# Performance work log

Measured on AMD Instinct MI355X. Metric: run time of the kernel, lower is better.

## Reference

```python
import jax, jax.numpy as jnp
import numpy as np

B, S, D, H = 4, 2048, 1024, 16
DK = D // H


def setup_inputs() -> dict:
    key = jax.random.key(0)
    ks = jax.random.split(key, 12)
    s = 1.0 / np.sqrt(D)
    return {
        "query": jax.random.normal(ks[0], (B, S, D), jnp.float32),
        "key": jax.random.normal(ks[1], (B, S, D), jnp.float32),
        "value": jax.random.normal(ks[2], (B, S, D), jnp.float32),
        "mask": jax.random.randint(ks[3], (B, S), 0, 2, jnp.int32),
        "wq": jax.random.normal(ks[4], (D, D), jnp.float32) * s,
        "bq": jnp.zeros((D,), jnp.float32),
        "wk": jax.random.normal(ks[5], (D, D), jnp.float32) * s,
        "bk": jnp.zeros((D,), jnp.float32),
        "wv": jax.random.normal(ks[6], (D, D), jnp.float32) * s,
        "bv": jnp.zeros((D,), jnp.float32),
        "wo": jax.random.normal(ks[7], (D, D), jnp.float32) * s,
        "bo": jnp.zeros((D,), jnp.float32),
    }


def reference(query, key, value, mask, wq, bq, wk, bk, wv, bv, wo, bo):
    # torch Linear: y = x @ W.T + b
    def proj(x, w, b):
        y = jnp.einsum('bsd,ed->bse', x, w) + b
        return y.reshape(B, S, H, DK).transpose(0, 2, 1, 3)  # [B,H,S,DK]

    q = proj(query, wq, bq)
    k = proj(key, wk, bk)
    v = proj(value, wv, bv)

    scores = jnp.einsum('bhqd,bhkd->bhqk', q, k) / jnp.sqrt(jnp.float32(DK))
    m = mask[:, None, None, :]  # [B,1,1,S_kv]
    scores = jnp.where(m == 0, jnp.float32(-1e9), scores)
    attn = jax.nn.softmax(scores, axis=-1)  # dropout p=0.0 (eval)
    out = jnp.einsum('bhqk,bhkd->bhqd', attn, v)
    out = out.transpose(0, 2, 1, 3).reshape(B, S, D)
    return jnp.einsum('bsd,ed->bse', out, wo) + bo
```

## Files before the change

### kernel.cpp

```cpp
#include <hip/hip_runtime.h>
#include <hip/hip_bf16.h>

typedef __bf16 bf16;
typedef bf16 bf16x2 __attribute__((ext_vector_type(2)));
typedef bf16 bf16x4 __attribute__((ext_vector_type(4)));
typedef bf16 bf16x8 __attribute__((ext_vector_type(8)));
typedef float f32x4 __attribute__((ext_vector_type(4)));
typedef float f32x16 __attribute__((ext_vector_type(16)));
typedef unsigned int u32;
typedef u32 u32x4 __attribute__((ext_vector_type(4)));

#define MFMA16(A,B,C) __builtin_amdgcn_mfma_f32_16x16x32_bf16(A,B,C,0,0,0)
#define MFMA32(A,B,C) __builtin_amdgcn_mfma_f32_32x32x16_bf16(A,B,C,0,0,0)

__device__ __forceinline__ void gld_lds16(const void* g, void* l) {
  __builtin_amdgcn_global_load_lds(
      (const __attribute__((address_space(1))) void*)g,
      (__attribute__((address_space(3))) void*)l, 16, 0, 0);
}

__global__ void cast3_kernel(const float* __restrict__ s0, const float* __restrict__ s1,
                             const float* __restrict__ s2,
                             bf16* __restrict__ d0, bf16* __restrict__ d1, bf16* __restrict__ d2) {
  const int which = blockIdx.x >> 13;
  const int i = (blockIdx.x & 8191) * 256 + threadIdx.x;
  const float* s = which == 0 ? s0 : which == 1 ? s1 : s2;
  bf16* d = which == 0 ? d0 : which == 1 ? d1 : d2;
  float4 v = ((const float4*)s)[i];
  bf16x4 o;
  o[0] = (bf16)v.x; o[1] = (bf16)v.y; o[2] = (bf16)v.z; o[3] = (bf16)v.w;
  *(bf16x4*)(d + (size_t)i * 4) = o;
}

__global__ void cast4_kernel(const float* __restrict__ s0, const float* __restrict__ s1,
                             const float* __restrict__ s2, const float* __restrict__ s3,
                             bf16* __restrict__ d0, bf16* __restrict__ d1,
                             bf16* __restrict__ d2, bf16* __restrict__ d3) {
  const int which = blockIdx.x >> 10;
  const int i = (blockIdx.x & 1023) * 256 + threadIdx.x;
  const float* s = which == 0 ? s0 : which == 1 ? s1 : which == 2 ? s2 : s3;
  bf16* d = which == 0 ? d0 : which == 1 ? d1 : which == 2 ? d2 : d3;
  float4 v = ((const float4*)s)[i];
  bf16x4 o;
  o[0] = (bf16)v.x; o[1] = (bf16)v.y; o[2] = (bf16)v.z; o[3] = (bf16)v.w;
  *(bf16x4*)(d + (size_t)i * 4) = o;
}

__device__ __forceinline__ void gemm256_core(
    const bf16* __restrict__ aBase, const bf16* __restrict__ bBase,
    bf16* sA, bf16* sB, f32x4 (&acc)[8][4])
{
  const int t = threadIdx.x;
  const int lane = t & 63, w = t >> 6;
  const int wr = w >> 2, wc = w & 3;
  const int c = lane & 15, g = lane >> 4;

  const int tl   = (t * 16) ^ (((t >> 3) & 7) << 4);
  const int srow = tl >> 6;
  const int scol = (tl & 63) >> 1;
  const int dstE = t * 8;

  auto stage = [&](int buf, int kt) {
#pragma unroll
    for (int r = 0; r < 2; ++r)
      gld_lds16(aBase + (size_t)(r * 128 + srow) * 1024 + kt * 32 + scol,
                &sA[buf * 8192 + r * 4096 + dstE]);
#pragma unroll
    for (int r = 0; r < 2; ++r)
      gld_lds16(bBase + (size_t)(r * 128 + srow) * 1024 + kt * 32 + scol,
                &sB[buf * 8192 + r * 4096 + dstE]);
  };

  auto rd = [&](const bf16* s, int row) -> bf16x8 {
    const int phys = (row * 64 + g * 16) ^ (((row >> 1) & 7) << 4);
    return *(const bf16x8*)((const char*)s + phys);
  };

  stage(0, 0);
  stage(1, 1);

#pragma unroll 1
  for (int kt = 0; kt < 32; ++kt) {
    __builtin_amdgcn_s_barrier();
    if (kt < 30) {
      stage((kt + 2) % 3, kt + 2);
      asm volatile("s_waitcnt vmcnt(8)" ::: "memory");
    } else if (kt == 30) {
      asm volatile("s_waitcnt vmcnt(4)" ::: "memory");
    } else {
      asm volatile("s_waitcnt vmcnt(0)" ::: "memory");
    }
    __builtin_amdgcn_s_barrier();

    const bf16* tA = sA + (kt % 3) * 8192;
    const bf16* tB = sB + (kt % 3) * 8192;

    bf16x8 bfr[4];
#pragma unroll
    for (int ni = 0; ni < 4; ++ni) bfr[ni] = rd(tB, wc * 64 + ni * 16 + c);
    bf16x8 af[4];
#pragma unroll
    for (int mi = 0; mi < 4; ++mi) af[mi] = rd(tA, wr * 128 + mi * 16 + c);
    __builtin_amdgcn_s_setprio(1);
#pragma unroll
    for (int mi = 0; mi < 4; ++mi)
#pragma unroll
      for (int ni = 0; ni < 4; ++ni)
        acc[mi][ni] = MFMA16(af[mi], bfr[ni], acc[mi][ni]);
    __builtin_amdgcn_s_setprio(0);
#pragma unroll
    for (int mi = 0; mi < 4; ++mi) af[mi] = rd(tA, wr * 128 + (mi + 4) * 16 + c);
    __builtin_amdgcn_s_setprio(1);
#pragma unroll
    for (int mi = 0; mi < 4; ++mi)
#pragma unroll
      for (int ni = 0; ni < 4; ++ni)
        acc[mi + 4][ni] = MFMA16(af[mi], bfr[ni], acc[mi + 4][ni]);
    __builtin_amdgcn_s_setprio(0);
  }
}

__global__ __launch_bounds__(512, 2) void qkv_gemm256(
    const bf16* __restrict__ qx, const bf16* __restrict__ kx, const bf16* __restrict__ vx,
    const bf16* __restrict__ wqb, const bf16* __restrict__ wkb, const bf16* __restrict__ wvb,
    const float* __restrict__ bq, const float* __restrict__ bk, const float* __restrict__ bv,
    bf16* __restrict__ qp, bf16* __restrict__ kp, bf16* __restrict__ vt, float qscale)
{
  __shared__ bf16 sA[3 * 8192];
  __shared__ bf16 sB[3 * 8192];
  const int z = blockIdx.z;
  const bf16* A   = z == 0 ? qx  : z == 1 ? kx  : vx;
  const bf16* Bm  = z == 0 ? wqb : z == 1 ? wkb : wvb;
  const float* bias = z == 0 ? bq : z == 1 ? bk : bv;
  const int bm = blockIdx.y, bn = blockIdx.x;

  f32x4 acc[8][4] = {};
  gemm256_core(A + (size_t)(bm * 256) * 1024, Bm + (size_t)(bn * 256) * 1024, sA, sB, acc);

  const int t = threadIdx.x, lane = t & 63, w = t >> 6;
  const int wr = w >> 2, wc = w & 3, c = lane & 15, g = lane >> 4;
  const float sc = z == 0 ? qscale : 1.0f;
  bf16* Cb = z == 0 ? qp : kp;
#pragma unroll
  for (int ni = 0; ni < 4; ++ni) {
    const int col = bn * 256 + wc * 64 + ni * 16 + c;
    const float bvv = bias[col];
#pragma unroll
    for (int mi = 0; mi < 8; ++mi) {
#pragma unroll
      for (int r4 = 0; r4 < 4; ++r4) {
        const int row = bm * 256 + wr * 128 + mi * 16 + g * 4 + r4;
        const float val = (acc[mi][ni][r4] + bvv) * sc;
        if (z == 2) {
          const int bb = row >> 11, s = row & 2047;
          vt[((size_t)(bb * 1024 + col)) * 2048 + s] = (bf16)val;
        } else {
          Cb[(size_t)row * 1024 + col] = (bf16)val;
        }
      }
    }
  }
}

__global__ __launch_bounds__(512, 2) void out_gemm256(
    const bf16* __restrict__ A, const bf16* __restrict__ Bm,
    const float* __restrict__ bias, float* __restrict__ Cout)
{
  __shared__ bf16 sA[3 * 8192];
  __shared__ bf16 sB[3 * 8192];
  const int bm = blockIdx.y, bn = blockIdx.x;

  f32x4 acc[8][4] = {};
  gemm256_core(A + (size_t)(bm * 256) * 1024, Bm + (size_t)(bn * 256) * 1024, sA, sB, acc);

  const int t = threadIdx.x, lane = t & 63, w = t >> 6;
  const int wr = w >> 2, wc = w & 3, c = lane & 15, g = lane >> 4;
#pragma unroll
  for (int ni = 0; ni < 4; ++ni) {
    const int col = bn * 256 + wc * 64 + ni * 16 + c;
    const float bvv = bias[col];
#pragma unroll
    for (int mi = 0; mi < 8; ++mi) {
#pragma unroll
      for (int r4 = 0; r4 < 4; ++r4) {
        const int row = bm * 256 + wr * 128 + mi * 16 + g * 4 + r4;
        Cout[(size_t)row * 1024 + col] = acc[mi][ni][r4] + bvv;
      }
    }
  }
}

__global__ __launch_bounds__(256) void attn_kernel(
    const bf16* __restrict__ Qp, const bf16* __restrict__ Kp, const bf16* __restrict__ Vt,
    const int* __restrict__ mask, bf16* __restrict__ Out)
{
  __shared__ bf16 sK[2][64 * 64];
  __shared__ bf16 sV[2][64 * 64];

  const int bh = blockIdx.x;
  const int b = bh >> 4, h = bh & 15;
  const int t = threadIdx.x, lane = t & 63, w = t >> 6;
  const int q32 = lane & 31, hi = lane >> 5;
  const int q0 = blockIdx.y * 128 + w * 32;

  const char* kBase = (const char*)(Kp + (size_t)(b * 2048) * 1024 + h * 64);
  const char* vBase = (const char*)(Vt + (size_t)(bh * 64) * 2048);

  auto stageKV = [&](int buf, int kt) {
#pragma unroll
    for (int i = 0; i < 2; ++i) {
      const int idx = i * 256 + t;
      const int row = idx >> 3;
      const int cb = ((t & 7) * 16) ^ ((row & 7) << 4);
      gld_lds16(kBase + (size_t)(kt * 64 + row) * 2048 + cb, (char*)sK[buf] + idx * 16);
      gld_lds16(vBase + (size_t)row * 4096 + kt * 128 + cb, (char*)sV[buf] + idx * 16);
    }
  };

  bf16x8 qf[4];
  const bf16* qrow = Qp + (size_t)(b * 2048 + q0 + q32) * 1024 + h * 64;
#pragma unroll
  for (int ks = 0; ks < 4; ++ks)
    qf[ks] = *(const bf16x8*)&qrow[ks * 16 + hi * 8];

  float mrun = -1e30f, lrun = 0.f;
  f32x16 aco[2] = {};

  const int* mrow = mask + b * 2048;

  stageKV(0, 0);
  __syncthreads();
  int cur = 0;
  for (int kt = 0; kt < 32; ++kt) {
    if (kt + 1 < 32) stageKV(cur ^ 1, kt + 1);

    f32x16 st[2];
#pragma unroll
    for (int kf = 0; kf < 2; ++kf)
#pragma unroll
      for (int q4 = 0; q4 < 4; ++q4) {
        const int4 mm = *(const int4*)&mrow[kt * 64 + kf * 32 + q4 * 8 + hi * 4];
        st[kf][q4 * 4 + 0] = mm.x ? 0.0f : -1e9f;
        st[kf][q4 * 4 + 1] = mm.y ? 0.0f : -1e9f;
        st[kf][q4 * 4 + 2] = mm.z ? 0.0f : -1e9f;
        st[kf][q4 * 4 + 3] = mm.w ? 0.0f : -1e9f;
      }

#pragma unroll
    for (int ks = 0; ks < 4; ++ks) {
      bf16x8 k0f, k1f;
      {
        const int row = q32;
        const int byt = (row * 128 + ks * 32 + hi * 16) ^ ((row & 7) << 4);
        k0f = *(const bf16x8*)((const char*)sK[cur] + byt);
      }
      {
        const int row = 32 + q32;
        const int byt = (row * 128 + ks * 32 + hi * 16) ^ ((row & 7) << 4);
        k1f = *(const bf16x8*)((const char*)sK[cur] + byt);
      }
      __builtin_amdgcn_s_setprio(1);
      st[0] = MFMA32(k0f, qf[ks], st[0]);
      st[1] = MFMA32(k1f, qf[ks], st[1]);
      __builtin_amdgcn_s_setprio(0);
    }

    float t0 = fmaxf(st[0][0], st[0][1]), t1 = fmaxf(st[0][2], st[0][3]);
    float t2 = fmaxf(st[1][0], st[1][1]), t3 = fmaxf(st[1][2], st[1][3]);
#pragma unroll
    for (int i = 4; i < 16; i += 4) {
      t0 = fmaxf(t0, fmaxf(st[0][i], st[0][i + 1]));
      t1 = fmaxf(t1, fmaxf(st[0][i + 2], st[0][i + 3]));
      t2 = fmaxf(t2, fmaxf(st[1][i], st[1][i + 1]));
      t3 = fmaxf(t3, fmaxf(st[1][i + 2], st[1][i + 3]));
    }
    float tmax = fmaxf(fmaxf(t0, t1), fmaxf(t2, t3));
    tmax = fmaxf(tmax, __shfl_xor(tmax, 32, 64));
    if (!__all(tmax <= mrun + 11.5f)) {
      const float mnew = fmaxf(mrun, tmax);
      const float sc = exp2f(mrun - mnew);
      mrun = mnew;
      lrun *= sc;
      aco[0] *= sc;
      aco[1] *= sc;
    }
    float rs0 = 0.f, rs1 = 0.f, rs2 = 0.f, rs3 = 0.f;
#pragma unroll
    for (int i = 0; i < 16; i += 4) {
      float p00 = exp2f(st[0][i] - mrun),     p01 = exp2f(st[0][i + 1] - mrun);
      float p02 = exp2f(st[0][i + 2] - mrun), p03 = exp2f(st[0][i + 3] - mrun);
      float p10 = exp2f(st[1][i] - mrun),     p11 = exp2f(st[1][i + 1] - mrun);
      float p12 = exp2f(st[1][i + 2] - mrun), p13 = exp2f(st[1][i + 3] - mrun);
      st[0][i] = p00; st[0][i + 1] = p01; st[0][i + 2] = p02; st[0][i + 3] = p03;
      st[1][i] = p10; st[1][i + 1] = p11; st[1][i + 2] = p12; st[1][i + 3] = p13;
      rs0 += p00 + p01; rs1 += p02 + p03;
      rs2 += p10 + p11; rs3 += p12 + p13;
    }
    float rs = (rs0 + rs1) + (rs2 + rs3);
    rs += __shfl_xor(rs, 32, 64);
    lrun += rs;

    bf16x8 pa[4];
#pragma unroll
    for (int kf = 0; kf < 2; ++kf) {
      u32 u[4][2];
#pragma unroll
      for (int g2 = 0; g2 < 4; ++g2) {
        asm("v_cvt_pk_bf16_f32 %0, %1, %2"
            : "=v"(u[g2][0]) : "v"(st[kf][4 * g2 + 0]), "v"(st[kf][4 * g2 + 1]));
        asm("v_cvt_pk_bf16_f32 %0, %1, %2"
            : "=v"(u[g2][1]) : "v"(st[kf][4 * g2 + 2]), "v"(st[kf][4 * g2 + 3]));
      }
      u32 d0 = u[0][0], d2 = u[1][0];
      asm("v_permlane32_swap_b32 %0, %1" : "+v"(d0), "+v"(d2));
      u32 d1 = u[0][1], d3 = u[1][1];
      asm("v_permlane32_swap_b32 %0, %1" : "+v"(d1), "+v"(d3));
      u32x4 ud = {d0, d1, d2, d3};
      pa[2 * kf] = __builtin_bit_cast(bf16x8, ud);
      u32 e0 = u[2][0], e2 = u[3][0];
      asm("v_permlane32_swap_b32 %0, %1" : "+v"(e0), "+v"(e2));
      u32 e1 = u[2][1], e3 = u[3][1];
      asm("v_permlane32_swap_b32 %0, %1" : "+v"(e1), "+v"(e3));
      u32x4 ue = {e0, e1, e2, e3};
      pa[2 * kf + 1] = __builtin_bit_cast(bf16x8, ue);
    }

#pragma unroll
    for (int kk = 0; kk < 4; ++kk) {
      bf16x8 vb0, vb1;
      {
        const int row = q32;
        const int byt = (row * 128 + kk * 32 + hi * 16) ^ ((row & 7) << 4);
        vb0 = *(const bf16x8*)((const char*)sV[cur] + byt);
      }
      {
        const int row = 32 + q32;
        const int byt = (row * 128 + kk * 32 + hi * 16) ^ ((row & 7) << 4);
        vb1 = *(const bf16x8*)((const char*)sV[cur] + byt);
      }
      __builtin_amdgcn_s_setprio(1);
      aco[0] = MFMA32(vb0, pa[kk], aco[0]);
      aco[1] = MFMA32(vb1, pa[kk], aco[1]);
      __builtin_amdgcn_s_setprio(0);
    }

    __syncthreads();
    cur ^= 1;
  }

  const float inv = 1.0f / lrun;
  bf16* orow = Out + (size_t)(b * 2048 + q0 + q32) * 1024 + h * 64;
#pragma unroll
  for (int dkf = 0; dkf < 2; ++dkf)
#pragma unroll
    for (int q4 = 0; q4 < 4; ++q4) {
      bf16x4 o;
#pragma unroll
      for (int r4 = 0; r4 < 4; ++r4)
        o[r4] = (bf16)(aco[dkf][q4 * 4 + r4] * inv);
      *(bf16x4*)&orow[dkf * 32 + q4 * 8 + hi * 4] = o;
    }
}

extern "C" void kernel_launch(void* const* d_in, const int* in_sizes, int n_in,
                              void* d_out, int out_size, void* d_ws, size_t ws_size,
                              hipStream_t stream) {
  const float* q  = (const float*)d_in[0];
  const float* k  = (const float*)d_in[1];
  const float* v  = (const float*)d_in[2];
  const int*  msk = (const int*)d_in[3];
  const float* wq = (const float*)d_in[4];
  const float* bq = (const float*)d_in[5];
  const float* wk = (const float*)d_in[6];
  const float* bk = (const float*)d_in[7];
  const float* wv = (const float*)d_in[8];
  const float* bv = (const float*)d_in[9];
  const float* wo = (const float*)d_in[10];
  const float* bo = (const float*)d_in[11];

  bf16* ws = (bf16*)d_ws;
  const size_t NEL = 8192ull * 1024ull;
  bf16* qx  = ws;
  bf16* kx  = ws + NEL;
  bf16* vx  = ws + 2 * NEL;
  bf16* wqb = ws + 3 * NEL;
  bf16* wkb = wqb + 1048576;
  bf16* wvb = wkb + 1048576;
  bf16* wob = wvb + 1048576;
  bf16* qp  = wob + 1048576;
  bf16* kp  = qp + NEL;
  bf16* vt  = kp + NEL;
  bf16* ao  = vx;

  cast3_kernel<<<24576, 256, 0, stream>>>(q, k, v, qx, kx, vx);
  cast4_kernel<<<4096, 256, 0, stream>>>(wq, wk, wv, wo, wqb, wkb, wvb, wob);

  const float qscale = 0.125f * 1.44269504088896f;
  qkv_gemm256<<<dim3(4, 32, 3), 512, 0, stream>>>(qx, kx, vx, wqb, wkb, wvb,
                                                  bq, bk, bv, qp, kp, vt, qscale);
  attn_kernel<<<dim3(64, 16), 256, 0, stream>>>(qp, kp, vt, msk, ao);
  out_gemm256<<<dim3(4, 32), 512, 0, stream>>>(ao, wob, bo, (float*)d_out);
}
```

Before: 495.1 us.

## Shrink GEMM tiles to 128x256 with double buffering and merge attention K/V LDS

The QKV and output GEMMs now use 128x256 tiles instead of 256x256, with double-buffered staging instead of triple, less LDS and fewer accumulators, and launch bounds raised to 4 blocks per CU. This doubles the grid so more blocks are in flight and more CUs stay busy, at the cost of lower per-block data reuse and a shallower prefetch pipeline. The attention kernel also merges its K and V shared tiles into one interleaved 256-byte-row buffer with a 16-way XOR swizzle, issuing four uniform async loads per thread.

After: 467.2 us. 1.06x faster.

```diff
diff --git a/kernel.cpp b/kernel.cpp
--- a/kernel.cpp
+++ b/kernel.cpp
@@ -48,27 +48,24 @@
 
 __device__ __forceinline__ void gemm256_core(
     const bf16* __restrict__ aBase, const bf16* __restrict__ bBase,
-    bf16* sA, bf16* sB, f32x4 (&acc)[8][4])
+    bf16* sA, bf16* sB, f32x4 (&acc)[4][4])
 {
   const int t = threadIdx.x;
   const int lane = t & 63, w = t >> 6;
   const int wr = w >> 2, wc = w & 3;
   const int c = lane & 15, g = lane >> 4;
 
-  const int tl   = (t * 16) ^ (((t >> 3) & 7) << 4);
-  const int srow = tl >> 6;
-  const int scol = (tl & 63) >> 1;
-  const int dstE = t * 8;
+  const int pA = t * 16;
+  const int lA = pA ^ (((pA >> 7) & 7) << 4);
+  const int srA = lA >> 6;
+  const int scA = (lA & 63) >> 1;
 
   auto stage = [&](int buf, int kt) {
+    gld_lds16(aBase + (size_t)srA * 1024 + kt * 32 + scA, &sA[buf * 4096 + t * 8]);
 #pragma unroll
     for (int r = 0; r < 2; ++r)
-      gld_lds16(aBase + (size_t)(r * 128 + srow) * 1024 + kt * 32 + scol,
-                &sA[buf * 8192 + r * 4096 + dstE]);
-#pragma unroll
-    for (int r = 0; r < 2; ++r)
-      gld_lds16(bBase + (size_t)(r * 128 + srow) * 1024 + kt * 32 + scol,
-                &sB[buf * 8192 + r * 4096 + dstE]);
+      gld_lds16(bBase + (size_t)(r * 128 + srA) * 1024 + kt * 32 + scA,
+                &sB[buf * 8192 + r * 4096 + t * 8]);
   };
 
   auto rd = [&](const bf16* s, int row) -> bf16x8 {
@@ -77,30 +74,25 @@
   };
 
   stage(0, 0);
-  stage(1, 1);
-
+  int buf = 0;
 #pragma unroll 1
   for (int kt = 0; kt < 32; ++kt) {
     __builtin_amdgcn_s_barrier();
-    if (kt < 30) {
-      stage((kt + 2) % 3, kt + 2);
-      asm volatile("s_waitcnt vmcnt(8)" ::: "memory");
-    } else if (kt == 30) {
-      asm volatile("s_waitcnt vmcnt(4)" ::: "memory");
+    if (kt < 31) {
+      stage(buf ^ 1, kt + 1);
+      asm volatile("s_waitcnt vmcnt(3)" ::: "memory");
     } else {
       asm volatile("s_waitcnt vmcnt(0)" ::: "memory");
     }
     __builtin_amdgcn_s_barrier();
 
-    const bf16* tA = sA + (kt % 3) * 8192;
-    const bf16* tB = sB + (kt % 3) * 8192;
-
-    bf16x8 bfr[4];
+    const bf16* tA = sA + buf * 4096;
+    const bf16* tB = sB + buf * 8192;
+    bf16x8 af[4], bfr[4];
+#pragma unroll
+    for (int mi = 0; mi < 4; ++mi) af[mi] = rd(tA, wr * 64 + mi * 16 + c);
 #pragma unroll
     for (int ni = 0; ni < 4; ++ni) bfr[ni] = rd(tB, wc * 64 + ni * 16 + c);
-    bf16x8 af[4];
-#pragma unroll
-    for (int mi = 0; mi < 4; ++mi) af[mi] = rd(tA, wr * 128 + mi * 16 + c);
     __builtin_amdgcn_s_setprio(1);
 #pragma unroll
     for (int mi = 0; mi < 4; ++mi)
@@ -108,34 +100,26 @@
       for (int ni = 0; ni < 4; ++ni)
         acc[mi][ni] = MFMA16(af[mi], bfr[ni], acc[mi][ni]);
     __builtin_amdgcn_s_setprio(0);
-#pragma unroll
-    for (int mi = 0; mi < 4; ++mi) af[mi] = rd(tA, wr * 128 + (mi + 4) * 16 + c);
-    __builtin_amdgcn_s_setprio(1);
-#pragma unroll
-    for (int mi = 0; mi < 4; ++mi)
-#pragma unroll
-      for (int ni = 0; ni < 4; ++ni)
-        acc[mi + 4][ni] = MFMA16(af[mi], bfr[ni], acc[mi + 4][ni]);
-    __builtin_amdgcn_s_setprio(0);
+    buf ^= 1;
   }
 }
 
-__global__ __launch_bounds__(512, 2) void qkv_gemm256(
+__global__ __launch_bounds__(512, 4) void qkv_gemm256(
     const bf16* __restrict__ qx, const bf16* __restrict__ kx, const bf16* __restrict__ vx,
     const bf16* __restrict__ wqb, const bf16* __restrict__ wkb, const bf16* __restrict__ wvb,
     const float* __restrict__ bq, const float* __restrict__ bk, const float* __restrict__ bv,
     bf16* __restrict__ qp, bf16* __restrict__ kp, bf16* __restrict__ vt, float qscale)
 {
-  __shared__ bf16 sA[3 * 8192];
-  __shared__ bf16 sB[3 * 8192];
+  __shared__ bf16 sA[2 * 4096];
+  __shared__ bf16 sB[2 * 8192];
   const int z = blockIdx.z;
   const bf16* A   = z == 0 ? qx  : z == 1 ? kx  : vx;
   const bf16* Bm  = z == 0 ? wqb : z == 1 ? wkb : wvb;
   const float* bias = z == 0 ? bq : z == 1 ? bk : bv;
   const int bm = blockIdx.y, bn = blockIdx.x;
 
-  f32x4 acc[8][4] = {};
-  gemm256_core(A + (size_t)(bm * 256) * 1024, Bm + (size_t)(bn * 256) * 1024, sA, sB, acc);
+  f32x4 acc[4][4] = {};
+  gemm256_core(A + (size_t)(bm * 128) * 1024, Bm + (size_t)(bn * 256) * 1024, sA, sB, acc);
 
   const int t = threadIdx.x, lane = t & 63, w = t >> 6;
   const int wr = w >> 2, wc = w & 3, c = lane & 15, g = lane >> 4;
@@ -146,10 +130,10 @@
     const int col = bn * 256 + wc * 64 + ni * 16 + c;
     const float bvv = bias[col];
 #pragma unroll
-    for (int mi = 0; mi < 8; ++mi) {
+    for (int mi = 0; mi < 4; ++mi) {
 #pragma unroll
       for (int r4 = 0; r4 < 4; ++r4) {
-        const int row = bm * 256 + wr * 128 + mi * 16 + g * 4 + r4;
+        const int row = bm * 128 + wr * 64 + mi * 16 + g * 4 + r4;
         const float val = (acc[mi][ni][r4] + bvv) * sc;
         if (z == 2) {
           const int bb = row >> 11, s = row & 2047;
@@ -162,16 +146,16 @@
   }
 }
 
-__global__ __launch_bounds__(512, 2) void out_gemm256(
+__global__ __launch_bounds__(512, 4) void out_gemm256(
     const bf16* __restrict__ A, const bf16* __restrict__ Bm,
     const float* __restrict__ bias, float* __restrict__ Cout)
 {
-  __shared__ bf16 sA[3 * 8192];
-  __shared__ bf16 sB[3 * 8192];
+  __shared__ bf16 sA[2 * 4096];
+  __shared__ bf16 sB[2 * 8192];
   const int bm = blockIdx.y, bn = blockIdx.x;
 
-  f32x4 acc[8][4] = {};
-  gemm256_core(A + (size_t)(bm * 256) * 1024, Bm + (size_t)(bn * 256) * 1024, sA, sB, acc);
+  f32x4 acc[4][4] = {};
+  gemm256_core(A + (size_t)(bm * 128) * 1024, Bm + (size_t)(bn * 256) * 1024, sA, sB, acc);
 
   const int t = threadIdx.x, lane = t & 63, w = t >> 6;
   const int wr = w >> 2, wc = w & 3, c = lane & 15, g = lane >> 4;
@@ -180,10 +164,10 @@
     const int col = bn * 256 + wc * 64 + ni * 16 + c;
     const float bvv = bias[col];
 #pragma unroll
-    for (int mi = 0; mi < 8; ++mi) {
+    for (int mi = 0; mi < 4; ++mi) {
 #pragma unroll
       for (int r4 = 0; r4 < 4; ++r4) {
-        const int row = bm * 256 + wr * 128 + mi * 16 + g * 4 + r4;
+        const int row = bm * 128 + wr * 64 + mi * 16 + g * 4 + r4;
         Cout[(size_t)row * 1024 + col] = acc[mi][ni][r4] + bvv;
       }
     }
@@ -194,8 +178,7 @@
     const bf16* __restrict__ Qp, const bf16* __restrict__ Kp, const bf16* __restrict__ Vt,
     const int* __restrict__ mask, bf16* __restrict__ Out)
 {
-  __shared__ bf16 sK[2][64 * 64];
-  __shared__ bf16 sV[2][64 * 64];
+  __shared__ bf16 sKV[2][64 * 128];
 
   const int bh = blockIdx.x;
   const int b = bh >> 4, h = bh & 15;
@@ -208,12 +191,15 @@
 
   auto stageKV = [&](int buf, int kt) {
 #pragma unroll
-    for (int i = 0; i < 2; ++i) {
-      const int idx = i * 256 + t;
-      const int row = idx >> 3;
-      const int cb = ((t & 7) * 16) ^ ((row & 7) << 4);
-      gld_lds16(kBase + (size_t)(kt * 64 + row) * 2048 + cb, (char*)sK[buf] + idx * 16);
-      gld_lds16(vBase + (size_t)row * 4096 + kt * 128 + cb, (char*)sV[buf] + idx * 16);
+    for (int j = 0; j < 4; ++j) {
+      const int P = j * 4096 + t * 16;
+      const int L = P ^ (((P >> 8) & 15) << 4);
+      const int row = L >> 8;
+      const int off = L & 255;
+      const char* src = (off < 128)
+          ? kBase + (size_t)(kt * 64 + row) * 2048 + off
+          : vBase + (size_t)row * 4096 + kt * 128 + (off - 128);
+      gld_lds16(src, (char*)sKV[buf] + P);
     }
   };
 
@@ -251,13 +237,13 @@
       bf16x8 k0f, k1f;
       {
         const int row = q32;
-        const int byt = (row * 128 + ks * 32 + hi * 16) ^ ((row & 7) << 4);
-        k0f = *(const bf16x8*)((const char*)sK[cur] + byt);
+        const int phys = row * 256 + ((ks * 32 + hi * 16) ^ ((row & 15) << 4));
+        k0f = *(const bf16x8*)((const char*)sKV[cur] + phys);
       }
       {
         const int row = 32 + q32;
-        const int byt = (row * 128 + ks * 32 + hi * 16) ^ ((row & 7) << 4);
-        k1f = *(const bf16x8*)((const char*)sK[cur] + byt);
+        const int phys = row * 256 + ((ks * 32 + hi * 16) ^ ((row & 15) << 4));
+        k1f = *(const bf16x8*)((const char*)sKV[cur] + phys);
       }
       __builtin_amdgcn_s_setprio(1);
       st[0] = MFMA32(k0f, qf[ks], st[0]);
@@ -330,13 +316,13 @@
       bf16x8 vb0, vb1;
       {
         const int row = q32;
-        const int byt = (row * 128 + kk * 32 + hi * 16) ^ ((row & 7) << 4);
-        vb0 = *(const bf16x8*)((const char*)sV[cur] + byt);
+        const int phys = row * 256 + ((128 + kk * 32 + hi * 16) ^ ((row & 15) << 4));
+        vb0 = *(const bf16x8*)((const char*)sKV[cur] + phys);
       }
       {
         const int row = 32 + q32;
-        const int byt = (row * 128 + kk * 32 + hi * 16) ^ ((row & 7) << 4);
-        vb1 = *(const bf16x8*)((const char*)sV[cur] + byt);
+        const int phys = row * 256 + ((128 + kk * 32 + hi * 16) ^ ((row & 15) << 4));
+        vb1 = *(const bf16x8*)((const char*)sKV[cur] + phys);
       }
       __builtin_amdgcn_s_setprio(1);
       aco[0] = MFMA32(vb0, pa[kk], aco[0]);
@@ -396,8 +382,8 @@
   cast4_kernel<<<4096, 256, 0, stream>>>(wq, wk, wv, wo, wqb, wkb, wvb, wob);
 
   const float qscale = 0.125f * 1.44269504088896f;
-  qkv_gemm256<<<dim3(4, 32, 3), 512, 0, stream>>>(qx, kx, vx, wqb, wkb, wvb,
+  qkv_gemm256<<<dim3(4, 64, 3), 512, 0, stream>>>(qx, kx, vx, wqb, wkb, wvb,
                                                   bq, bk, bv, qp, kp, vt, qscale);
   attn_kernel<<<dim3(64, 16), 256, 0, stream>>>(qp, kp, vt, msk, ao);
-  out_gemm256<<<dim3(4, 32), 512, 0, stream>>>(ao, wob, bo, (float*)d_out);
-}
+  out_gemm256<<<dim3(4, 64), 512, 0, stream>>>(ao, wob, bo, (float*)d_out);
+}
```
